# Optimization experiments

Measured on AMD Instinct MI355X. Metric: run time of the kernel, lower is better.

Reference implementation:

```python
import jax, jax.numpy as jnp
import numpy as np

GRID = 112  # densepose predictor output resolution (hardcoded in forward)
D = 16      # CSE embedding dim (view(16, -1) in forward)


def setup_inputs() -> dict:
    key = jax.random.key(0)
    k1, k2 = jax.random.split(key)
    feats = jax.random.normal(k1, (2, D, GRID, GRID), dtype=jnp.float32)
    vertex_embeddings = jax.random.normal(k2, (27554, D), dtype=jnp.float32)
    return {"feats": feats, "vertex_embeddings": vertex_embeddings}


def reference(feats, vertex_embeddings):
    # feats: [B, 16, 112, 112]; vertex_embeddings: [M, 16]
    B = feats.shape[0]
    # per-pixel embeddings: [B, N, D] with N = 112*112 (matches feats[i].view(16,-1).T)
    x = feats.reshape(B, D, -1).transpose(0, 2, 1)
    x2 = jnp.sum(x * x, axis=-1, keepdims=True)            # [B, N, 1]
    v2 = jnp.sum(vertex_embeddings * vertex_embeddings, -1)  # [M]
    dist = x2 - 2.0 * jnp.einsum('bnd,md->bnm', x, vertex_embeddings) + v2
    dps = jnp.argmin(dist, axis=-1).reshape(B, GRID, GRID)  # [B, 112, 112] int
    return feats, dps
```

## Files before the change

### kernel.cpp

```cpp
#include <hip/hip_runtime.h>
#include <math.h>
#include <float.h>

#define GRIDP 112
#define NPIX (GRIDP * GRIDP)
#define D 16
#define TSA 3328
#define TSB 3072
#define G 2
#define TG 4
#define GRPB (TG * TSA)
#define NISS (GRPB / 1024)

typedef short s16x8 __attribute__((ext_vector_type(8)));
typedef float f32x16 __attribute__((ext_vector_type(16)));
typedef unsigned int uint32;
typedef const __attribute__((address_space(1))) uint32* gas_ptr;
typedef __attribute__((address_space(3))) uint32* las_ptr;

__device__ inline unsigned short f2bf(float x) {
    unsigned u = __float_as_uint(x);
    u += 0x7fffu + ((u >> 16) & 1u);
    return (unsigned short)(u >> 16);
}
__device__ inline float bf2f(unsigned short b) { return __uint_as_float(((unsigned)b) << 16); }

#define MFMA __builtin_amdgcn_mfma_f32_32x32x16_bf16

__global__ __launch_bounds__(256) void prep_fused(
    const float* __restrict__ verts, const float* __restrict__ feats,
    char* __restrict__ abuf, char* __restrict__ bbuf,
    float* __restrict__ v2p, float* __restrict__ outf,
    int M, int Mtiles, int NP, int PTiles, int nvb, int npb, int nf4)
{
    int bx = blockIdx.x;
    if (bx < nvb) {
        int mp = bx * 256 + threadIdx.x;
        if (mp >= Mtiles * 32) return;
        int tile = mp >> 5, row = mp & 31;
        float x[D]; float v2;
        if (mp < M) {
            const float4* r4 = (const float4*)(verts + (size_t)mp * D);
            float4 a = r4[0], b = r4[1], c = r4[2], d = r4[3];
            x[0]=a.x; x[1]=a.y; x[2]=a.z; x[3]=a.w;
            x[4]=b.x; x[5]=b.y; x[6]=b.z; x[7]=b.w;
            x[8]=c.x; x[9]=c.y; x[10]=c.z; x[11]=c.w;
            x[12]=d.x; x[13]=d.y; x[14]=d.z; x[15]=d.w;
            float s = 0.f;
#pragma unroll
            for (int e = 0; e < D; ++e) s = fmaf(x[e], x[e], s);
            v2 = s;
            v2p[mp] = s;
        } else {
#pragma unroll
            for (int e = 0; e < D; ++e) x[e] = 0.f;
            v2 = FLT_MAX;
        }
        size_t tb = (size_t)tile * TSA;
        int hv = (row >> 2) & 1, rv = (row & 3) + 4 * (row >> 3);
        *(float*)(abuf + tb + 3072 + hv * 64 + rv * 4) = v2;
#pragma unroll
        for (int e = 0; e < D; ++e) {
            float v = x[e];
            unsigned short t0 = f2bf(v);  float r1 = v - bf2f(t0);
            unsigned short t1 = f2bf(r1); float r2 = r1 - bf2f(t1);
            unsigned short t2 = f2bf(r2);
            size_t o = tb + (size_t)(e >> 3) * 512 + (size_t)row * 16 + (size_t)(e & 7) * 2;
            *(unsigned short*)(abuf + o)        = t0;
            *(unsigned short*)(abuf + o + 1024) = t1;
            *(unsigned short*)(abuf + o + 2048) = t2;
        }
    } else if (bx < nvb + npb) {
        int p = (bx - nvb) * 256 + threadIdx.x;
        if (p >= PTiles * 32) return;
        int tile = p >> 5, colr = p & 31;
        float x[D];
        if (p < NP) {
            int b = p / NPIX, n = p - b * NPIX;
            const float* xf = feats + ((size_t)b * D) * NPIX + n;
#pragma unroll
            for (int e = 0; e < D; ++e) x[e] = -2.0f * xf[(size_t)e * NPIX];
        } else {
#pragma unroll
            for (int e = 0; e < D; ++e) x[e] = 0.f;
        }
        size_t tb = (size_t)tile * TSB;
#pragma unroll
        for (int e = 0; e < D; ++e) {
            float v = x[e];
            unsigned short t0 = f2bf(v);  float r1 = v - bf2f(t0);
            unsigned short t1 = f2bf(r1); float r2 = r1 - bf2f(t1);
            unsigned short t2 = f2bf(r2);
            size_t o = tb + (size_t)(e >> 3) * 512 + (size_t)colr * 16 + (size_t)(e & 7) * 2;
            *(unsigned short*)(bbuf + o)        = t0;
            *(unsigned short*)(bbuf + o + 1024) = t1;
            *(unsigned short*)(bbuf + o + 2048) = t2;
        }
    } else {
        int i = (bx - nvb - npb) * 256 + threadIdx.x;
        if (i < nf4)
            ((float4*)outf)[i] = ((const float4*)feats)[i];
    }
}

__device__ inline float mintree16(const f32x16& a) {
    float a0 = fminf(fminf(a[0],  a[1]),  a[2]);
    float a1 = fminf(fminf(a[3],  a[4]),  a[5]);
    float a2 = fminf(fminf(a[6],  a[7]),  a[8]);
    float a3 = fminf(fminf(a[9],  a[10]), a[11]);
    float a4 = fminf(fminf(a[12], a[13]), a[14]);
    float a5 = fminf(fminf(a0, a1), a[15]);
    float a6 = fminf(fminf(a2, a3), a4);
    return fminf(a5, a6);
}

__device__ __forceinline__ void stage_group(const char* gbase, char* lbase,
                                            int wid, int lane) {
    for (int i = wid; i < NISS; i += 4) {
        __builtin_amdgcn_global_load_lds(
            (gas_ptr)(gbase + i * 1024 + lane * 16),
            (las_ptr)(lbase + i * 1024),
            16, 0, 0);
    }
}

__global__ __launch_bounds__(256) void mfma_scan(
    const char* __restrict__ abuf, const char* __restrict__ bbuf,
    float* __restrict__ pval, int* __restrict__ ptile,
    int Mtiles, int chunk, int NP, int PTiles)
{
    __shared__ __align__(16) char smem[2][GRPB];
    int lane = threadIdx.x & 63;
    int wid  = threadIdx.x >> 6;
    int col  = lane & 31, h = lane >> 5;
    int ptb  = (blockIdx.x * 4 + wid) * G;

    s16x8 bh[G], bm[G], bl[G];
#pragma unroll
    for (int g = 0; g < G; ++g) {
        int pt = ptb + g;
        int ptc = pt < PTiles ? pt : PTiles - 1;
        const char* bb = bbuf + (size_t)ptc * TSB + (size_t)h * 512 + (size_t)col * 16;
        bh[g] = *(const s16x8*)bb;
        bm[g] = *(const s16x8*)(bb + 1024);
        bl[g] = *(const s16x8*)(bb + 2048);
    }

    int mt0 = blockIdx.y * chunk;
    int mt1 = mt0 + chunk; if (mt1 > Mtiles) mt1 = Mtiles;
    int nT   = mt1 - mt0;
    int nGrp = (nT + TG - 1) / TG;

    float best[G]; int btl[G];
#pragma unroll
    for (int g = 0; g < G; ++g) { best[g] = FLT_MAX; btl[g] = mt0; }

    const char* gsrc = abuf + (size_t)mt0 * TSA;

    stage_group(gsrc, smem[0], wid, lane);
    __syncthreads();

    int cur = 0;
    for (int grp = 0; grp < nGrp; ++grp) {
        if (grp + 1 < nGrp)
            stage_group(gsrc + (size_t)(grp + 1) * GRPB, smem[cur ^ 1], wid, lane);

        const char* lb = smem[cur];
        int tmax = nT - grp * TG; if (tmax > TG) tmax = TG;
        for (int t = 0; t < tmax; ++t) {
            const char* lt = lb + t * TSA;
            s16x8 ah = *(const s16x8*)(lt + (size_t)h * 512 + (size_t)col * 16);
            s16x8 am = *(const s16x8*)(lt + 1024 + (size_t)h * 512 + (size_t)col * 16);
            s16x8 al = *(const s16x8*)(lt + 2048 + (size_t)h * 512 + (size_t)col * 16);
            f32x16 c = *(const f32x16*)(lt + 3072 + (size_t)h * 64);

            f32x16 acc[G];
#pragma unroll
            for (int g = 0; g < G; ++g) acc[g] = MFMA(ah, bh[g], c, 0, 0, 0);
#pragma unroll
            for (int g = 0; g < G; ++g) acc[g] = MFMA(ah, bm[g], acc[g], 0, 0, 0);
#pragma unroll
            for (int g = 0; g < G; ++g) acc[g] = MFMA(am, bh[g], acc[g], 0, 0, 0);
#pragma unroll
            for (int g = 0; g < G; ++g) acc[g] = MFMA(ah, bl[g], acc[g], 0, 0, 0);
#pragma unroll
            for (int g = 0; g < G; ++g) acc[g] = MFMA(am, bm[g], acc[g], 0, 0, 0);
#pragma unroll
            for (int g = 0; g < G; ++g) acc[g] = MFMA(al, bh[g], acc[g], 0, 0, 0);

            int mt = mt0 + grp * TG + t;
#pragma unroll
            for (int g = 0; g < G; ++g) {
                float m = mintree16(acc[g]);
                if (m < best[g]) { btl[g] = mt; best[g] = m; }
            }
        }
        __syncthreads();
        cur ^= 1;
    }

#pragma unroll
    for (int g = 0; g < G; ++g) {
        float o = __shfl_xor(best[g], 32, 64);
        int  ot = __shfl_xor(btl[g], 32, 64);
        if (o < best[g] || (o == best[g] && ot < btl[g])) { best[g] = o; btl[g] = ot; }
    }
    if (lane < 32) {
        int s = blockIdx.y;
#pragma unroll
        for (int g = 0; g < G; ++g) {
            int pt = ptb + g;
            int px = pt * 32 + col;
            if (pt < PTiles && px < NP) {
                pval[(size_t)s * NP + px] = best[g];
                ptile[(size_t)s * NP + px] = btl[g];
            }
        }
    }
}

__global__ __launch_bounds__(256) void finalize(
    const float* __restrict__ pval, const int* __restrict__ ptile,
    const float* __restrict__ feats, const float* __restrict__ verts,
    const float* __restrict__ v2p, float* __restrict__ dps,
    int S, int NP, int M)
{
    int p = blockIdx.x * 256 + threadIdx.x;
    if (p >= NP) return;
    float bv = pval[p]; int bt = ptile[p];
    for (int s = 1; s < S; ++s) {
        float v = pval[(size_t)s * NP + p];
        int   t = ptile[(size_t)s * NP + p];
        if (v < bv || (v == bv && t < bt)) { bv = v; bt = t; }
    }
    int b = p / NPIX, n = p - b * NPIX;
    const float* xf = feats + ((size_t)b * D) * NPIX + n;
    float xs[D];
#pragma unroll
    for (int d2 = 0; d2 < D; ++d2) xs[d2] = -2.0f * xf[(size_t)d2 * NPIX];
    int m0 = bt * 32, m1 = m0 + 32; if (m1 > M) m1 = M;
    float best = FLT_MAX; int bi = m0;
    for (int m = m0; m < m1; ++m) {
        const float4* vr = (const float4*)(verts + (size_t)m * D);
        float4 a = vr[0], bq = vr[1], c = vr[2], d = vr[3];
        float acc = v2p[m];
        acc = fmaf(a.x, xs[0], acc);  acc = fmaf(a.y, xs[1], acc);
        acc = fmaf(a.z, xs[2], acc);  acc = fmaf(a.w, xs[3], acc);
        acc = fmaf(bq.x, xs[4], acc); acc = fmaf(bq.y, xs[5], acc);
        acc = fmaf(bq.z, xs[6], acc); acc = fmaf(bq.w, xs[7], acc);
        acc = fmaf(c.x, xs[8], acc);  acc = fmaf(c.y, xs[9], acc);
        acc = fmaf(c.z, xs[10], acc); acc = fmaf(c.w, xs[11], acc);
        acc = fmaf(d.x, xs[12], acc); acc = fmaf(d.y, xs[13], acc);
        acc = fmaf(d.z, xs[14], acc); acc = fmaf(d.w, xs[15], acc);
        if (acc < best) { best = acc; bi = m; }
    }
    dps[p] = (float)bi;
}

__global__ __launch_bounds__(256) void v2_kernel(const float* __restrict__ verts,
                                                 float* __restrict__ v2, int M) {
    int m = blockIdx.x * 256 + threadIdx.x;
    if (m >= M) return;
    const float4* r = (const float4*)(verts + (size_t)m * D);
    float4 a = r[0], b = r[1], c = r[2], d = r[3];
    v2[m] = ((a.x*a.x + a.y*a.y) + (a.z*a.z + a.w*a.w))
          + ((b.x*b.x + b.y*b.y) + (b.z*b.z + b.w*b.w))
          + ((c.x*c.x + c.y*c.y) + (c.z*c.z + c.w*c.w))
          + ((d.x*d.x + d.y*d.y) + (d.z*d.z + d.w*d.w));
}

__global__ __launch_bounds__(256) void argmin_partial(
    const float* __restrict__ feats, const float* __restrict__ verts,
    const float* __restrict__ v2, float* __restrict__ pval, int* __restrict__ pidx,
    int M, int NPtot, int chunk)
{
    int p = blockIdx.x * 256 + threadIdx.x;
    if (p >= NPtot) return;
    int b = p / NPIX, n = p - b * NPIX;
    const float* xf = feats + ((size_t)b * D) * NPIX + n;
    float x[D];
#pragma unroll
    for (int d2 = 0; d2 < D; ++d2) x[d2] = -2.0f * xf[(size_t)d2 * NPIX];
    int s = blockIdx.y;
    int m0 = s * chunk, m1 = m0 + chunk; if (m1 > M) m1 = M;
    float best = INFINITY; int bi = 0;
    for (int m = m0; m < m1; ++m) {
        const float* vr = verts + (size_t)m * D;
        float acc = v2[m];
#pragma unroll
        for (int d2 = 0; d2 < D; ++d2) acc = fmaf(vr[d2], x[d2], acc);
        if (acc < best) { best = acc; bi = m; }
    }
    pval[(size_t)s * NPtot + p] = best;
    pidx[(size_t)s * NPtot + p] = bi;
}

__global__ __launch_bounds__(256) void reduce_idx(
    const float* __restrict__ pval, const int* __restrict__ pidx,
    float* __restrict__ dps, int S, int NP)
{
    int p = blockIdx.x * 256 + threadIdx.x;
    if (p >= NP) return;
    float bv = pval[p]; int bi = pidx[p];
    for (int s = 1; s < S; ++s) {
        float v = pval[(size_t)s * NP + p];
        int   i = pidx[(size_t)s * NP + p];
        if (v < bv || (v == bv && i < bi)) { bv = v; bi = i; }
    }
    dps[p] = (float)bi;
}

extern "C" void kernel_launch(void* const* d_in, const int* in_sizes, int n_in,
                              void* d_out, int out_size, void* d_ws, size_t ws_size,
                              hipStream_t stream)
{
    const float* feats = (const float*)d_in[0];
    const float* verts = (const float*)d_in[1];
    int M          = in_sizes[1] / D;
    int feat_elems = in_sizes[0];
    int Bn         = feat_elems / (D * NPIX);
    int NP         = Bn * NPIX;
    float* out = (float*)d_out;

    int PTiles = (NP + 31) >> 5;
    int Mtiles = (M + 31) >> 5;

    size_t off = 0;
    auto alloc = [&](size_t sz) { size_t o = off; off = (off + sz + 255) & ~(size_t)255; return o; };
    size_t oBF = alloc((size_t)PTiles * TSB);
    size_t oAF = alloc((size_t)(Mtiles + 8) * TSA);
    size_t oV2 = alloc((size_t)M * 4);
    size_t base = off;

    int S = 32;
    while (S > 1 && base + (size_t)S * NP * 8 > ws_size) S >>= 1;

    if (base + (size_t)S * NP * 8 <= ws_size) {
        char*  bbuf = (char*)d_ws + oBF;
        char*  abuf = (char*)d_ws + oAF;
        float* v2p  = (float*)((char*)d_ws + oV2);
        float* pval = (float*)((char*)d_ws + base);
        int*   ptil = (int*)((char*)d_ws + base + (size_t)S * NP * 4);

        int nvb = (Mtiles * 32 + 255) / 256;
        int npb = (PTiles * 32 + 255) / 256;
        int nf4 = feat_elems / 4;
        int ncb = (nf4 + 255) / 256;
        prep_fused<<<dim3(nvb + npb + ncb), dim3(256), 0, stream>>>(
            verts, feats, abuf, bbuf, v2p, out, M, Mtiles, NP, PTiles, nvb, npb, nf4);

        int chunk = (Mtiles + S - 1) / S;
        mfma_scan<<<dim3((PTiles + 4 * G - 1) / (4 * G), S), dim3(256), 0, stream>>>(
            abuf, bbuf, pval, ptil, Mtiles, chunk, NP, PTiles);

        finalize<<<dim3((NP + 255) / 256), dim3(256), 0, stream>>>(
            pval, ptil, feats, verts, v2p, out + feat_elems, S, NP, M);
    } else {
        hipMemcpyAsync(out, feats, (size_t)feat_elems * sizeof(float),
                       hipMemcpyDeviceToDevice, stream);
        char* ws = (char*)d_ws;
        float* v2 = (float*)ws;
        size_t o2 = (((size_t)M * 4) + 255) & ~(size_t)255;
        int S2 = 16;
        while (S2 > 1 && o2 + (size_t)S2 * NP * 8 > ws_size) S2 >>= 1;
        float* pval = (float*)(ws + o2);
        int*   pidx = (int*)(ws + o2 + (size_t)S2 * NP * 4);
        int chunk = (M + S2 - 1) / S2;
        v2_kernel<<<dim3((M + 255) / 256), dim3(256), 0, stream>>>(verts, v2, M);
        argmin_partial<<<dim3((NP + 255) / 256, S2), dim3(256), 0, stream>>>(
            feats, verts, v2, pval, pidx, M, NP, chunk);
        reduce_idx<<<dim3((NP + 255) / 256), dim3(256), 0, stream>>>(
            pval, pidx, out + feat_elems, S2, NP);
    }
}
```

Measured before the change: 151.0 us.

## Vectorize split-bf16 stores in prep and double vertex tile group size

```diff
diff --git a/kernel.cpp b/kernel.cpp
--- a/kernel.cpp
+++ b/kernel.cpp
@@ -8,7 +8,7 @@
 #define TSA 3328
 #define TSB 3072
 #define G 2
-#define TG 4
+#define TG 8
 #define GRPB (TG * TSA)
 #define NISS (GRPB / 1024)
 
@@ -26,6 +26,31 @@
 __device__ inline float bf2f(unsigned short b) { return __uint_as_float(((unsigned)b) << 16); }
 
 #define MFMA __builtin_amdgcn_mfma_f32_32x32x16_bf16
+
+__device__ __forceinline__ void split_store_row(const float* x, char* base, int row) {
+    unsigned short t0[D], t1[D], t2[D];
+#pragma unroll
+    for (int e = 0; e < D; ++e) {
+        float v = x[e];
+        unsigned short a = f2bf(v);  float r1 = v - bf2f(a);
+        unsigned short b = f2bf(r1); float r2 = r1 - bf2f(b);
+        t0[e] = a; t1[e] = b; t2[e] = f2bf(r2);
+    }
+#pragma unroll
+    for (int h2 = 0; h2 < 2; ++h2) {
+        char* p = base + h2 * 512 + row * 16;
+        s16x8 v0, v1, v2s;
+#pragma unroll
+        for (int j = 0; j < 8; ++j) {
+            v0[j] = (short)t0[h2 * 8 + j];
+            v1[j] = (short)t1[h2 * 8 + j];
+            v2s[j] = (short)t2[h2 * 8 + j];
+        }
+        *(s16x8*)(p)        = v0;
+        *(s16x8*)(p + 1024) = v1;
+        *(s16x8*)(p + 2048) = v2s;
+    }
+}
 
 __global__ __launch_bounds__(256) void prep_fused(
     const float* __restrict__ verts, const float* __restrict__ feats,
@@ -59,17 +84,7 @@
         size_t tb = (size_t)tile * TSA;
         int hv = (row >> 2) & 1, rv = (row & 3) + 4 * (row >> 3);
         *(float*)(abuf + tb + 3072 + hv * 64 + rv * 4) = v2;
-#pragma unroll
-        for (int e = 0; e < D; ++e) {
-            float v = x[e];
-            unsigned short t0 = f2bf(v);  float r1 = v - bf2f(t0);
-            unsigned short t1 = f2bf(r1); float r2 = r1 - bf2f(t1);
-            unsigned short t2 = f2bf(r2);
-            size_t o = tb + (size_t)(e >> 3) * 512 + (size_t)row * 16 + (size_t)(e & 7) * 2;
-            *(unsigned short*)(abuf + o)        = t0;
-            *(unsigned short*)(abuf + o + 1024) = t1;
-            *(unsigned short*)(abuf + o + 2048) = t2;
-        }
+        split_store_row(x, abuf + tb, row);
     } else if (bx < nvb + npb) {
         int p = (bx - nvb) * 256 + threadIdx.x;
         if (p >= PTiles * 32) return;
@@ -84,18 +99,7 @@
 #pragma unroll
             for (int e = 0; e < D; ++e) x[e] = 0.f;
         }
-        size_t tb = (size_t)tile * TSB;
-#pragma unroll
-        for (int e = 0; e < D; ++e) {
-            float v = x[e];
-            unsigned short t0 = f2bf(v);  float r1 = v - bf2f(t0);
-            unsigned short t1 = f2bf(r1); float r2 = r1 - bf2f(t1);
-            unsigned short t2 = f2bf(r2);
-            size_t o = tb + (size_t)(e >> 3) * 512 + (size_t)colr * 16 + (size_t)(e & 7) * 2;
-            *(unsigned short*)(bbuf + o)        = t0;
-            *(unsigned short*)(bbuf + o + 1024) = t1;
-            *(unsigned short*)(bbuf + o + 2048) = t2;
-        }
+        split_store_row(x, bbuf + (size_t)tile * TSB, colr);
     } else {
         int i = (bx - nvb - npb) * 256 + threadIdx.x;
         if (i < nf4)
@@ -328,7 +332,7 @@
     size_t off = 0;
     auto alloc = [&](size_t sz) { size_t o = off; off = (off + sz + 255) & ~(size_t)255; return o; };
     size_t oBF = alloc((size_t)PTiles * TSB);
-    size_t oAF = alloc((size_t)(Mtiles + 8) * TSA);
+    size_t oAF = alloc((size_t)(Mtiles + 2 * TG) * TSA);
     size_t oV2 = alloc((size_t)M * 4);
     size_t base = off;
 
```

Result: no change. 151.9 us (+0.6%).
